# Performance work log

Hardware: AMD Instinct MI355X
Metric: run time of the kernel (lower is better)

The kernel has to match this reference:

```python
import jax, jax.numpy as jnp
import numpy as np

B, S, H, NH = 4, 1024, 1024, 16
HD = H // NH
I = 4096
EPS = 1e-12
BASE = 10000.0


def setup_inputs() -> dict:
    key = jax.random.key(0)
    ks = jax.random.split(key, 6)
    sc = 0.02
    return {
        "x": jax.random.normal(ks[0], (B, S, H), jnp.float32),
        "ln1_w": jnp.ones((H,), jnp.float32),
        "ln1_b": jnp.zeros((H,), jnp.float32),
        "qkv_w": jax.random.normal(ks[1], (3 * H, H), jnp.float32) * sc,
        "qkv_b": jnp.zeros((3 * H,), jnp.float32),
        "out_w": jax.random.normal(ks[2], (H, H), jnp.float32) * sc,
        "out_b": jnp.zeros((H,), jnp.float32),
        "ln2_w": jnp.ones((H,), jnp.float32),
        "ln2_b": jnp.zeros((H,), jnp.float32),
        "i2h_w": jax.random.normal(ks[3], (2 * I, H), jnp.float32) * sc,
        "i2h_b": jnp.zeros((2 * I,), jnp.float32),
        "h2o_w": jax.random.normal(ks[4], (H, I), jnp.float32) * sc,
        "h2o_b": jnp.zeros((H,), jnp.float32),
    }


def _layer_norm(x, w, b, eps=EPS):
    mu = jnp.mean(x, axis=-1, keepdims=True)
    var = jnp.mean(jnp.square(x - mu), axis=-1, keepdims=True)
    return (x - mu) * jax.lax.rsqrt(var + eps) * w + b


def _rope_cos_sin(seq_len, dim, base):
    # inv_freq = base ** linspace(0, -1 + 2/dim, dim//2), repeated twice
    half = jnp.power(base, jnp.linspace(0.0, -1.0 + 2.0 / dim, dim // 2, dtype=jnp.float32))
    inv_freq = jnp.concatenate([half, half])  # [dim]
    t = jnp.arange(seq_len, dtype=jnp.float32)
    freqs = t[:, None] * inv_freq[None, :]  # [seq, dim]
    return jnp.cos(freqs), jnp.sin(freqs)


def _rotate(x, cos, sin):
    # x: [B, NH, S, HD]; cos/sin: [S, HD]
    xl, xr = jnp.split(x, 2, axis=-1)
    x_rot = jnp.concatenate([-xr, xl], axis=-1)
    return x * cos + x_rot * sin


def _forward(x, ln1_w, ln1_b, qkv_w, qkv_b, out_w, out_b,
             ln2_w, ln2_b, i2h_w, i2h_b, h2o_w, h2o_b):
    b, s, h = x.shape
    # --- LeanSelfAttention (pre-LN, rotary, causal, residual) ---
    h_ln = _layer_norm(x, ln1_w, ln1_b)
    qkv = h_ln @ qkv_w.T + qkv_b  # [b, s, 3h]
    q, k, v = jnp.split(qkv, 3, axis=-1)
    to_heads = lambda t: t.reshape(b, s, NH, HD).transpose(0, 2, 1, 3)  # [b,nh,s,hd]
    q, k, v = to_heads(q), to_heads(k), to_heads(v)
    cos, sin = _rope_cos_sin(s, HD, BASE)
    q, k = _rotate(q, cos, sin), _rotate(k, cos, sin)
    scores = jnp.einsum("bhqd,bhkd->bhqk", q, k) / np.sqrt(HD).astype(np.float32)
    causal = jnp.tril(jnp.ones((s, s), dtype=bool))
    scores = jnp.where(causal, scores, jnp.float32(-10000.0))
    probs = jax.nn.softmax(scores, axis=-1)
    attn = jnp.einsum("bhqk,bhkd->bhqd", probs, v)
    attn = attn.transpose(0, 2, 1, 3).reshape(b, s, h)
    attn_out = attn @ out_w.T + out_b + x  # residual
    # --- LeanFFN (pre-LN, gated gelu, residual) ---
    ffn_ln = _layer_norm(attn_out, ln2_w, ln2_b)
    pre = ffn_ln @ i2h_w.T + i2h_b  # [b, s, 2I]
    gate, lin = jnp.split(pre, 2, axis=-1)
    hid = jax.nn.gelu(gate, approximate=False) * lin
    return hid @ h2o_w.T + h2o_b + attn_out


def reference(x, ln1_w, ln1_b, qkv_w, qkv_b, out_w, out_b,
              ln2_w, ln2_b, i2h_w, i2h_b, h2o_w, h2o_b):
    return _forward(x, ln1_w, ln1_b, qkv_w, qkv_b, out_w, out_b,
                    ln2_w, ln2_b, i2h_w, i2h_b, h2o_w, h2o_b)
```

## Files before the change

kernel.cpp:

```cpp
#include <hip/hip_runtime.h>
#include <cstdint>
#include <cstddef>

typedef __bf16 bf16;
typedef __bf16 bf16x4 __attribute__((ext_vector_type(4)));
typedef __bf16 bf16x8 __attribute__((ext_vector_type(8)));
typedef float  f32x4  __attribute__((ext_vector_type(4)));

#define GLD16(gptr, lptr)                                                      \
  __builtin_amdgcn_global_load_lds(                                            \
      (__attribute__((address_space(1))) unsigned int*)(gptr),                 \
      (__attribute__((address_space(3))) unsigned int*)(lptr), 16, 0, 0)

__global__ __launch_bounds__(256)
void convert_kernel(const float* __restrict__ src, bf16* __restrict__ dst, int n8)
{
    const int j = blockIdx.x * 256 + threadIdx.x;
    if (j >= n8) return;
    const float* s = src + (size_t)j * 8;
    bf16x8 o;
#pragma unroll
    for (int e = 0; e < 8; ++e) o[e] = (bf16)s[e];
    ((bf16x8*)dst)[j] = o;
}

template<class InT>
__global__ __launch_bounds__(256)
void ln_kernel(const InT* __restrict__ x, const float* __restrict__ w,
               const float* __restrict__ b, bf16* __restrict__ out)
{
    __shared__ float red[8];
    const int row = blockIdx.x;
    const int tid = threadIdx.x;
    const InT* xr = x + (size_t)row * 1024;
    float xf[4], s = 0.f, ss = 0.f;
#pragma unroll
    for (int j = 0; j < 4; ++j) {
        xf[j] = (float)xr[tid * 4 + j];
        s += xf[j]; ss += xf[j] * xf[j];
    }
#pragma unroll
    for (int off = 32; off > 0; off >>= 1) { s += __shfl_xor(s, off); ss += __shfl_xor(ss, off); }
    if ((tid & 63) == 0) { red[(tid >> 6) * 2] = s; red[(tid >> 6) * 2 + 1] = ss; }
    __syncthreads();
    s  = red[0] + red[2] + red[4] + red[6];
    ss = red[1] + red[3] + red[5] + red[7];
    const float mu   = s * (1.f / 1024.f);
    const float var  = ss * (1.f / 1024.f) - mu * mu;
    const float rstd = rsqrtf(var + 1e-12f);
    bf16x4 ov;
#pragma unroll
    for (int j = 0; j < 4; ++j)
        ov[j] = (bf16)((xf[j] - mu) * rstd * w[tid * 4 + j] + b[tid * 4 + j]);
    *(bf16x4*)(out + (size_t)row * 1024 + tid * 4) = ov;
}

template<int RES_MODE, bool OUT_F32>
__global__ __launch_bounds__(256)
void gemm_bt(const bf16* __restrict__ A, const bf16* __restrict__ W,
             const float* __restrict__ bias, const void* __restrict__ res,
             void* __restrict__ Cv, int M, int N, int K)
{
    __shared__ alignas(16) bf16 As[128][32];
    __shared__ alignas(16) bf16 Bs[128][32];
    const int tid  = threadIdx.x;
    const int lane = tid & 63, wid = tid >> 6;
    const int lr = lane & 15, lg = lane >> 4;
    const int kgrp = lg * 8;
    const int wm = (wid >> 1) * 64, wn = (wid & 1) * 64;
    const int row0 = blockIdx.x * 128, col0 = blockIdx.y * 128;

    f32x4 acc[4][4] = {};

    for (int k0 = 0; k0 < K; k0 += 32) {
#pragma unroll
        for (int i = 0; i < 2; ++i) {
            const int c = i * 256 + tid;
            const int r = c >> 2, k8 = (c & 3) * 8;
            GLD16(A + (size_t)(row0 + r) * K + k0 + k8,
                  (char*)&As[0][0] + (size_t)(i * 256 + wid * 64) * 16);
            GLD16(W + (size_t)(col0 + r) * K + k0 + k8,
                  (char*)&Bs[0][0] + (size_t)(i * 256 + wid * 64) * 16);
        }
        __syncthreads();
        bf16x8 af[4], bw[4];
#pragma unroll
        for (int mi = 0; mi < 4; ++mi) af[mi] = *(const bf16x8*)&As[wm + mi * 16 + lr][kgrp];
#pragma unroll
        for (int ni = 0; ni < 4; ++ni) bw[ni] = *(const bf16x8*)&Bs[wn + ni * 16 + lr][kgrp];
#pragma unroll
        for (int mi = 0; mi < 4; ++mi)
#pragma unroll
            for (int ni = 0; ni < 4; ++ni)
                acc[mi][ni] = __builtin_amdgcn_mfma_f32_16x16x32_bf16(
                    af[mi], bw[ni], acc[mi][ni], 0, 0, 0);
        __syncthreads();
    }

#pragma unroll
    for (int ni = 0; ni < 4; ++ni) {
        const int ccol = col0 + wn + ni * 16 + lr;
        const float bv = bias[ccol];
#pragma unroll
        for (int mi = 0; mi < 4; ++mi)
#pragma unroll
            for (int r = 0; r < 4; ++r) {
                const size_t crow = (size_t)(row0 + wm + mi * 16 + lg * 4 + r);
                float v = acc[mi][ni][r] + bv;
                if constexpr (RES_MODE == 1) v += ((const float*)res)[crow * N + ccol];
                if constexpr (RES_MODE == 2) v += (float)((const bf16*)res)[crow * N + ccol];
                if constexpr (OUT_F32) ((float*)Cv)[crow * N + ccol] = v;
                else                   ((bf16*)Cv)[crow * N + ccol] = (bf16)v;
            }
    }
}

__global__ __launch_bounds__(256)
void gemm_qkv_rope(const bf16* __restrict__ A, const bf16* __restrict__ W,
                   const float* __restrict__ bias, bf16* __restrict__ q_r,
                   bf16* __restrict__ k_r, bf16* __restrict__ v_r)
{
    __shared__ alignas(16) bf16 As[128][32];
    __shared__ alignas(16) bf16 Bs[128][32];
    const int tid  = threadIdx.x;
    const int lane = tid & 63, wid = tid >> 6;
    const int lr = lane & 15, lg = lane >> 4;
    const int kgrp = lg * 8;
    const int wm = (wid >> 1) * 64, wn = (wid & 1) * 64;
    const int row0 = blockIdx.x * 128, col0 = blockIdx.y * 128;
    const int K = 1024;

    f32x4 acc[4][4] = {};

    for (int k0 = 0; k0 < K; k0 += 32) {
#pragma unroll
        for (int i = 0; i < 2; ++i) {
            const int c = i * 256 + tid;
            const int r = c >> 2, k8 = (c & 3) * 8;
            GLD16(A + (size_t)(row0 + r) * K + k0 + k8,
                  (char*)&As[0][0] + (size_t)(i * 256 + wid * 64) * 16);
            GLD16(W + (size_t)(col0 + r) * K + k0 + k8,
                  (char*)&Bs[0][0] + (size_t)(i * 256 + wid * 64) * 16);
        }
        __syncthreads();
        bf16x8 af[4], bw[4];
#pragma unroll
        for (int mi = 0; mi < 4; ++mi) af[mi] = *(const bf16x8*)&As[wm + mi * 16 + lr][kgrp];
#pragma unroll
        for (int ni = 0; ni < 4; ++ni) bw[ni] = *(const bf16x8*)&Bs[wn + ni * 16 + lr][kgrp];
#pragma unroll
        for (int mi = 0; mi < 4; ++mi)
#pragma unroll
            for (int ni = 0; ni < 4; ++ni)
                acc[mi][ni] = __builtin_amdgcn_mfma_f32_16x16x32_bf16(
                    af[mi], bw[ni], acc[mi][ni], 0, 0, 0);
        __syncthreads();
    }

    const int third = blockIdx.y >> 3;
    bf16* dst = (third == 0) ? q_r : (third == 1) ? k_r : v_r;
#pragma unroll
    for (int ni = 0; ni < 2; ++ni) {
        const int i_ = ni * 16 + lr;
        const int ccol = col0 + wn + ni * 16 + lr;
        const int h = (ccol >> 6) & 15;
        const float blo = bias[ccol], bhi = bias[ccol + 32];
        const float inv = __expf((float)i_ * (-9.210340371976184f / 32.f));
#pragma unroll
        for (int mi = 0; mi < 4; ++mi)
#pragma unroll
            for (int r = 0; r < 4; ++r) {
                const int crow = row0 + wm + mi * 16 + lg * 4 + r;
                const int s = crow & 1023, b = crow >> 10;
                const float lo = acc[mi][ni][r] + blo;
                const float hi = acc[mi][ni + 2][r] + bhi;
                const size_t ob = ((size_t)(b * 16 + h) * 1024 + s) * 64;
                if (third == 2) {
                    dst[ob + i_]      = (bf16)lo;
                    dst[ob + i_ + 32] = (bf16)hi;
                } else {
                    float sn, c;
                    sincosf((float)s * inv, &sn, &c);
                    dst[ob + i_]      = (bf16)(lo * c - hi * sn);
                    dst[ob + i_ + 32] = (bf16)(hi * c + lo * sn);
                }
            }
    }
}

__global__ __launch_bounds__(512, 2)
void gemm_i2h_g8(const bf16* __restrict__ A, const bf16* __restrict__ W,
                 const float* __restrict__ bias, bf16* __restrict__ hid)
{
    __shared__ alignas(16) char smem[3 * 32768];
    const int tid  = threadIdx.x;
    const int lane = tid & 63, wid = tid >> 6;
    const int lrr  = lane & 15, lg = lane >> 4;
    const int wr = wid >> 2, wc = wid & 3;
    const int row0 = blockIdx.x * 256;
    const int colh = blockIdx.y * 128 + wc * 32;
    const int NT = 32;

    const int cA0 = tid, cA1 = 512 + tid;
    const int rA0 = cA0 >> 2, rA1 = cA1 >> 2, rB = tid >> 2;
    const int swA0 = (((cA0 & 3) * 16) ^ (((rA0 >> 1) & 3) << 4)) >> 1;
    const int swA1 = (((cA1 & 3) * 16) ^ (((rA1 >> 1) & 3) << 4)) >> 1;
    const int swB  = (((tid & 3) * 16) ^ (((rB  >> 1) & 3) << 4)) >> 1;
    const bf16* gA0 = A + (size_t)(row0 + rA0) * 1024 + swA0;
    const bf16* gA1 = A + (size_t)(row0 + rA1) * 1024 + swA1;
    const bf16* gBg = W + (size_t)(blockIdx.y * 128 + rB) * 1024 + swB;
    const bf16* gBl = W + (size_t)(4096 + blockIdx.y * 128 + rB) * 1024 + swB;
    const int dA0 = (wid * 64) * 16, dA1 = (512 + wid * 64) * 16, dB = (wid * 64) * 16;

    f32x4 acc[8][4] = {};

    {
        char* b0 = smem;
        GLD16(gBg, b0 + 16384 + dB); GLD16(gBl, b0 + 24576 + dB);
        GLD16(gA0, b0 + dA0);        GLD16(gA1, b0 + dA1);
        char* b1 = smem + 32768;
        GLD16(gBg + 32, b1 + 16384 + dB); GLD16(gBl + 32, b1 + 24576 + dB);
        GLD16(gA0 + 32, b1 + dA0);        GLD16(gA1 + 32, b1 + dA1);
    }
    asm volatile("s_waitcnt vmcnt(4)\ns_barrier" ::: "memory");

    int cur = 0, stg = 2;
    for (int t = 0; t < NT; ++t) {
        const char* bA  = smem + cur * 32768;
        const char* bBg = bA + 16384;
        const char* bBl = bA + 24576;
        char* sB = smem + stg * 32768;
        const int k0s = (t + 2) * 32;
        const bool dostg = (t < NT - 2);

        if (dostg) { GLD16(gBg + k0s, sB + 16384 + dB); GLD16(gBl + k0s, sB + 24576 + dB); }
        bf16x8 bf[4], af[4];
        const int bcol = lg * 16;
#pragma unroll
        for (int nv = 0; nv < 4; ++nv) {
            const int row = wc * 32 + (nv & 1) * 16 + lrr;
            const char* base = (nv < 2) ? bBg : bBl;
            bf[nv] = *(const bf16x8*)(base + row * 64 + (bcol ^ (((row >> 1) & 3) << 4)));
        }
#pragma unroll
        for (int mi = 0; mi < 4; ++mi) {
            const int row = wr * 128 + mi * 16 + lrr;
            af[mi] = *(const bf16x8*)(bA + row * 64 + (bcol ^ (((row >> 1) & 3) << 4)));
        }
        __builtin_amdgcn_s_barrier();
        __builtin_amdgcn_s_setprio(1);
#pragma unroll
        for (int mi = 0; mi < 4; ++mi)
#pragma unroll
            for (int nv = 0; nv < 4; ++nv)
                acc[mi][nv] = __builtin_amdgcn_mfma_f32_16x16x32_bf16(
                    af[mi], bf[nv], acc[mi][nv], 0, 0, 0);
        __builtin_amdgcn_s_setprio(0);
        __builtin_amdgcn_s_barrier();

        if (dostg) { GLD16(gA0 + k0s, sB + dA0); GLD16(gA1 + k0s, sB + dA1); }
#pragma unroll
        for (int mi = 0; mi < 4; ++mi) {
            const int row = wr * 128 + (4 + mi) * 16 + lrr;
            af[mi] = *(const bf16x8*)(bA + row * 64 + (bcol ^ (((row >> 1) & 3) << 4)));
        }
        __builtin_amdgcn_s_barrier();
        __builtin_amdgcn_s_setprio(1);
#pragma unroll
        for (int mi = 0; mi < 4; ++mi)
#pragma unroll
            for (int nv = 0; nv < 4; ++nv)
                acc[4 + mi][nv] = __builtin_amdgcn_mfma_f32_16x16x32_bf16(
                    af[mi], bf[nv], acc[4 + mi][nv], 0, 0, 0);
        __builtin_amdgcn_s_setprio(0);

        if (dostg) asm volatile("s_waitcnt vmcnt(4)\ns_barrier" ::: "memory");
        else       asm volatile("s_waitcnt vmcnt(0)\ns_barrier" ::: "memory");
        cur = (cur == 2) ? 0 : cur + 1;
        stg = (stg == 2) ? 0 : stg + 1;
    }

#pragma unroll
    for (int c = 0; c < 2; ++c) {
        const int gcol = colh + c * 16 + lrr;
        const float bg_ = bias[gcol], bl_ = bias[4096 + gcol];
#pragma unroll
        for (int mi = 0; mi < 8; ++mi)
#pragma unroll
            for (int r = 0; r < 4; ++r) {
                const size_t row = (size_t)(row0 + wr * 128 + mi * 16 + lg * 4 + r);
                const float g = acc[mi][c][r] + bg_;
                const float l = acc[mi][2 + c][r] + bl_;
                const float ge = 0.5f * g * (1.f + erff(g * 0.70710678118654752f));
                hid[row * 4096 + gcol] = (bf16)(ge * l);
            }
    }
}

__global__ __launch_bounds__(256)
void attn_kernel(const bf16* __restrict__ q_r, const bf16* __restrict__ k_r,
                 const bf16* __restrict__ v_r, bf16* __restrict__ attn)
{
    __shared__ alignas(16) bf16 Ks[64][72];
    __shared__ alignas(16) bf16 Vt[64][72];
    __shared__ alignas(16) bf16 Ps[4][16][72];
    const int qt = blockIdx.x, bh = blockIdx.y;
    const int tid = threadIdx.x, lane = tid & 63, w = tid >> 6;
    const int lr = lane & 15, lg = lane >> 4;
    const int kgrp = lg * 8;
    const int qbase = qt * 64;

    const bf16* qrow = q_r + ((size_t)bh * 1024 + qbase + w * 16 + lr) * 64;
    const bf16x8 qf0 = *(const bf16x8*)(qrow + kgrp);
    const bf16x8 qf1 = *(const bf16x8*)(qrow + 32 + kgrp);

    f32x4 o[4] = {};
    float m_r[4], l_r[4];
#pragma unroll
    for (int r = 0; r < 4; ++r) { m_r[r] = -1e30f; l_r[r] = 0.f; }

    const int nchunk = qt + 1;
    for (int ic = 0; ic < nchunk; ++ic) {
        const int kb = ic * 64;
        __syncthreads();
#pragma unroll
        for (int i = 0; i < 2; ++i) {
            const int c = i * 256 + tid;
            const int row = c >> 3, e8 = (c & 7) * 8;
            *(bf16x8*)&Ks[row][e8] =
                *(const bf16x8*)(k_r + ((size_t)bh * 1024 + kb + row) * 64 + e8);
            const bf16x8 vv =
                *(const bf16x8*)(v_r + ((size_t)bh * 1024 + kb + row) * 64 + e8);
#pragma unroll
            for (int j = 0; j < 8; ++j) Vt[e8 + j][row] = vv[j];
        }
        __syncthreads();

        f32x4 sv[4] = {};
#pragma unroll
        for (int nb = 0; nb < 4; ++nb) {
            const bf16x8 kf0 = *(const bf16x8*)&Ks[nb * 16 + lr][kgrp];
            const bf16x8 kf1 = *(const bf16x8*)&Ks[nb * 16 + lr][32 + kgrp];
            sv[nb] = __builtin_amdgcn_mfma_f32_16x16x32_bf16(qf0, kf0, sv[nb], 0, 0, 0);
            sv[nb] = __builtin_amdgcn_mfma_f32_16x16x32_bf16(qf1, kf1, sv[nb], 0, 0, 0);
        }

        const bool diag = (kb == qbase);
        float pv[4][4];
#pragma unroll
        for (int r = 0; r < 4; ++r) {
            float s0[4];
#pragma unroll
            for (int nb = 0; nb < 4; ++nb) {
                float t = sv[nb][r] * 0.125f;
                if (diag && (nb * 16 + lr) > (w * 16 + lg * 4 + r)) t = -10000.f;
                s0[nb] = t;
            }
            float rm = fmaxf(fmaxf(s0[0], s0[1]), fmaxf(s0[2], s0[3]));
#pragma unroll
            for (int off = 1; off < 16; off <<= 1) rm = fmaxf(rm, __shfl_xor(rm, off));
            const float nm = fmaxf(m_r[r], rm);
            const float sc = __expf(m_r[r] - nm);
            float rs = 0.f;
#pragma unroll
            for (int nb = 0; nb < 4; ++nb) {
                const float p = __expf(s0[nb] - nm);
                pv[nb][r] = p; rs += p;
            }
#pragma unroll
            for (int off = 1; off < 16; off <<= 1) rs += __shfl_xor(rs, off);
            l_r[r] = l_r[r] * sc + rs;
            m_r[r] = nm;
#pragma unroll
            for (int nb = 0; nb < 4; ++nb) o[nb][r] *= sc;
        }

#pragma unroll
        for (int nb = 0; nb < 4; ++nb)
#pragma unroll
            for (int r = 0; r < 4; ++r)
                Ps[w][lg * 4 + r][nb * 16 + lr] = (bf16)pv[nb][r];
#pragma unroll
        for (int nb = 0; nb < 4; ++nb)
#pragma unroll
            for (int ks = 0; ks < 2; ++ks) {
                const bf16x8 pa = *(const bf16x8*)&Ps[w][lr][ks * 32 + kgrp];
                const bf16x8 vb = *(const bf16x8*)&Vt[nb * 16 + lr][ks * 32 + kgrp];
                o[nb] = __builtin_amdgcn_mfma_f32_16x16x32_bf16(pa, vb, o[nb], 0, 0, 0);
            }
    }

    const int b = bh >> 4, head = bh & 15;
#pragma unroll
    for (int nb = 0; nb < 4; ++nb)
#pragma unroll
        for (int r = 0; r < 4; ++r) {
            const size_t rw = (size_t)(b * 1024 + qbase + w * 16 + lg * 4 + r);
            attn[rw * 1024 + head * 64 + nb * 16 + lr] = (bf16)(o[nb][r] / l_r[r]);
        }
}

extern "C" void kernel_launch(void* const* d_in, const int* in_sizes, int n_in,
                              void* d_out, int out_size, void* d_ws, size_t ws_size,
                              hipStream_t stream)
{
    const float* x    = (const float*)d_in[0];
    const float* ln1w = (const float*)d_in[1];
    const float* ln1b = (const float*)d_in[2];
    const float* qkvw = (const float*)d_in[3];
    const float* qkvb = (const float*)d_in[4];
    const float* outw = (const float*)d_in[5];
    const float* outb = (const float*)d_in[6];
    const float* ln2w = (const float*)d_in[7];
    const float* ln2b = (const float*)d_in[8];
    const float* i2hw = (const float*)d_in[9];
    const float* i2hb = (const float*)d_in[10];
    const float* h2ow = (const float*)d_in[11];
    const float* h2ob = (const float*)d_in[12];

    char* ws = (char*)d_ws;
    const size_t MB = 1024 * 1024;

    bf16* h_ln    = (bf16*)(ws + 0);
    bf16* q_r     = (bf16*)(ws + 8 * MB);
    bf16* k_r     = (bf16*)(ws + 16 * MB);
    bf16* v_r     = (bf16*)(ws + 24 * MB);
    bf16* attn    = (bf16*)(ws + 32 * MB);
    bf16* attnout = (bf16*)(ws + 40 * MB);
    bf16* ffnln   = (bf16*)(ws + 48 * MB);
    bf16* hid     = (bf16*)(ws + 56 * MB);
    bf16* qkvw_c  = (bf16*)(ws + 88 * MB);
    bf16* outw_c  = (bf16*)(ws + 94 * MB);
    bf16* i2hw_c  = (bf16*)(ws + 96 * MB);
    bf16* h2ow_c  = (bf16*)(ws + 112 * MB);

    convert_kernel<<<1536, 256, 0, stream>>>(qkvw, qkvw_c, 3145728 / 8);
    convert_kernel<<< 512, 256, 0, stream>>>(outw, outw_c, 1048576 / 8);
    convert_kernel<<<4096, 256, 0, stream>>>(i2hw, i2hw_c, 8388608 / 8);
    convert_kernel<<<2048, 256, 0, stream>>>(h2ow, h2ow_c, 4194304 / 8);

    ln_kernel<float><<<4096, 256, 0, stream>>>(x, ln1w, ln1b, h_ln);
    gemm_qkv_rope<<<dim3(32, 24), 256, 0, stream>>>(h_ln, qkvw_c, qkvb,
                                                    q_r, k_r, v_r);
    attn_kernel<<<dim3(16, 64), 256, 0, stream>>>(q_r, k_r, v_r, attn);
    gemm_bt<1, false><<<dim3(32, 8), 256, 0, stream>>>(
        attn, outw_c, outb, x, attnout, 4096, 1024, 1024);
    ln_kernel<bf16><<<4096, 256, 0, stream>>>(attnout, ln2w, ln2b, ffnln);
    gemm_i2h_g8<<<dim3(16, 32), 512, 0, stream>>>(ffnln, i2hw_c, i2hb, hid);
    gemm_bt<2, true><<<dim3(32, 8), 256, 0, stream>>>(
        hid, h2ow_c, h2ob, attnout, d_out, 4096, 1024, 4096);
}
```

Before: 484.9 us.

## Split-K the h2o GEMM into four partial passes plus a reduction kernel

The final h2o projection (K=4096) previously ran on a 32x8 grid of only 256 blocks. It is now split along K into four 1024-wide slices written as fp32 partials, followed by a reduction kernel that adds bias and residual. This raises block count to 1024 to fill more CUs, at the cost of 64MB of partial writes and reads. It also folds the 1/sqrt(d) scale into Q inside the QKV epilogue, removing a multiply per score in attention.

```diff
diff --git a/kernel.cpp b/kernel.cpp
--- a/kernel.cpp
+++ b/kernel.cpp
@@ -116,6 +116,83 @@
 }
 
 __global__ __launch_bounds__(256)
+void gemm_h2o_sk(const bf16* __restrict__ A, const bf16* __restrict__ W,
+                 float* __restrict__ part)
+{
+    __shared__ alignas(16) bf16 As[128][32];
+    __shared__ alignas(16) bf16 Bs[128][32];
+    const int tid  = threadIdx.x;
+    const int lane = tid & 63, wid = tid >> 6;
+    const int lr = lane & 15, lg = lane >> 4;
+    const int kgrp = lg * 8;
+    const int wm = (wid >> 1) * 64, wn = (wid & 1) * 64;
+    const int row0 = blockIdx.x * 128, col0 = blockIdx.y * 128;
+    const int kbase = blockIdx.z * 1024;
+    const int K = 4096;
+
+    f32x4 acc[4][4] = {};
+
+    for (int k0 = kbase; k0 < kbase + 1024; k0 += 32) {
+#pragma unroll
+        for (int i = 0; i < 2; ++i) {
+            const int c = i * 256 + tid;
+            const int r = c >> 2, k8 = (c & 3) * 8;
+            GLD16(A + (size_t)(row0 + r) * K + k0 + k8,
+                  (char*)&As[0][0] + (size_t)(i * 256 + wid * 64) * 16);
+            GLD16(W + (size_t)(col0 + r) * K + k0 + k8,
+                  (char*)&Bs[0][0] + (size_t)(i * 256 + wid * 64) * 16);
+        }
+        __syncthreads();
+        bf16x8 af[4], bw[4];
+#pragma unroll
+        for (int mi = 0; mi < 4; ++mi) af[mi] = *(const bf16x8*)&As[wm + mi * 16 + lr][kgrp];
+#pragma unroll
+        for (int ni = 0; ni < 4; ++ni) bw[ni] = *(const bf16x8*)&Bs[wn + ni * 16 + lr][kgrp];
+#pragma unroll
+        for (int mi = 0; mi < 4; ++mi)
+#pragma unroll
+            for (int ni = 0; ni < 4; ++ni)
+                acc[mi][ni] = __builtin_amdgcn_mfma_f32_16x16x32_bf16(
+                    af[mi], bw[ni], acc[mi][ni], 0, 0, 0);
+        __syncthreads();
+    }
+
+    float* dst = part + (size_t)blockIdx.z * 4096 * 1024;
+#pragma unroll
+    for (int ni = 0; ni < 4; ++ni) {
+        const int ccol = col0 + wn + ni * 16 + lr;
+#pragma unroll
+        for (int mi = 0; mi < 4; ++mi)
+#pragma unroll
+            for (int r = 0; r < 4; ++r) {
+                const size_t crow = (size_t)(row0 + wm + mi * 16 + lg * 4 + r);
+                dst[crow * 1024 + ccol] = acc[mi][ni][r];
+            }
+    }
+}
+
+__global__ __launch_bounds__(256)
+void h2o_reduce(const float* __restrict__ part, const float* __restrict__ bias,
+                const bf16* __restrict__ res, float* __restrict__ out)
+{
+    const size_t g = ((size_t)blockIdx.x * 256 + threadIdx.x) * 4;
+    const int col = (int)(g & 1023);
+    f32x4 v = *(const f32x4*)(part + g);
+#pragma unroll
+    for (int s = 1; s < 4; ++s) {
+        const f32x4 p = *(const f32x4*)(part + (size_t)s * 4096 * 1024 + g);
+#pragma unroll
+        for (int j = 0; j < 4; ++j) v[j] += p[j];
+    }
+    const f32x4 bv = *(const f32x4*)(bias + col);
+    const bf16x4 rv = *(const bf16x4*)(res + g);
+    f32x4 o;
+#pragma unroll
+    for (int j = 0; j < 4; ++j) o[j] = v[j] + bv[j] + (float)rv[j];
+    *(f32x4*)(out + g) = o;
+}
+
+__global__ __launch_bounds__(256)
 void gemm_qkv_rope(const bf16* __restrict__ A, const bf16* __restrict__ W,
                    const float* __restrict__ bias, bf16* __restrict__ q_r,
                    bf16* __restrict__ k_r, bf16* __restrict__ v_r)
@@ -159,6 +236,7 @@
 
     const int third = blockIdx.y >> 3;
     bf16* dst = (third == 0) ? q_r : (third == 1) ? k_r : v_r;
+    const float qs = (third == 0) ? 0.125f : 1.f;
 #pragma unroll
     for (int ni = 0; ni < 2; ++ni) {
         const int i_ = ni * 16 + lr;
@@ -181,8 +259,8 @@
                 } else {
                     float sn, c;
                     sincosf((float)s * inv, &sn, &c);
-                    dst[ob + i_]      = (bf16)(lo * c - hi * sn);
-                    dst[ob + i_ + 32] = (bf16)(hi * c + lo * sn);
+                    dst[ob + i_]      = (bf16)((lo * c - hi * sn) * qs);
+                    dst[ob + i_ + 32] = (bf16)((hi * c + lo * sn) * qs);
                 }
             }
     }
@@ -352,7 +430,7 @@
             float s0[4];
 #pragma unroll
             for (int nb = 0; nb < 4; ++nb) {
-                float t = sv[nb][r] * 0.125f;
+                float t = sv[nb][r];
                 if (diag && (nb * 16 + lr) > (w * 16 + lg * 4 + r)) t = -10000.f;
                 s0[nb] = t;
             }
@@ -421,18 +499,19 @@
     char* ws = (char*)d_ws;
     const size_t MB = 1024 * 1024;
 
-    bf16* h_ln    = (bf16*)(ws + 0);
-    bf16* q_r     = (bf16*)(ws + 8 * MB);
-    bf16* k_r     = (bf16*)(ws + 16 * MB);
-    bf16* v_r     = (bf16*)(ws + 24 * MB);
-    bf16* attn    = (bf16*)(ws + 32 * MB);
-    bf16* attnout = (bf16*)(ws + 40 * MB);
-    bf16* ffnln   = (bf16*)(ws + 48 * MB);
-    bf16* hid     = (bf16*)(ws + 56 * MB);
-    bf16* qkvw_c  = (bf16*)(ws + 88 * MB);
-    bf16* outw_c  = (bf16*)(ws + 94 * MB);
-    bf16* i2hw_c  = (bf16*)(ws + 96 * MB);
-    bf16* h2ow_c  = (bf16*)(ws + 112 * MB);
+    bf16*  h_ln    = (bf16*)(ws + 0);
+    bf16*  q_r     = (bf16*)(ws + 8 * MB);
+    bf16*  k_r     = (bf16*)(ws + 16 * MB);
+    bf16*  v_r     = (bf16*)(ws + 24 * MB);
+    bf16*  attn    = (bf16*)(ws + 32 * MB);
+    bf16*  ffnln   = (bf16*)(ws + 40 * MB);
+    float* part    = (float*)(ws + 0);
+    bf16*  attnout = (bf16*)(ws + 64 * MB);
+    bf16*  hid     = (bf16*)(ws + 72 * MB);
+    bf16*  qkvw_c  = (bf16*)(ws + 104 * MB);
+    bf16*  outw_c  = (bf16*)(ws + 110 * MB);
+    bf16*  i2hw_c  = (bf16*)(ws + 112 * MB);
+    bf16*  h2ow_c  = (bf16*)(ws + 128 * MB);
 
     convert_kernel<<<1536, 256, 0, stream>>>(qkvw, qkvw_c, 3145728 / 8);
     convert_kernel<<< 512, 256, 0, stream>>>(outw, outw_c, 1048576 / 8);
@@ -447,6 +526,6 @@
         attn, outw_c, outb, x, attnout, 4096, 1024, 1024);
     ln_kernel<bf16><<<4096, 256, 0, stream>>>(attnout, ln2w, ln2b, ffnln);
     gemm_i2h_g8<<<dim3(16, 32), 512, 0, stream>>>(ffnln, i2hw_c, i2hb, hid);
-    gemm_bt<2, true><<<dim3(32, 8), 256, 0, stream>>>(
-        hid, h2ow_c, h2ob, attnout, d_out, 4096, 1024, 4096);
-}
+    gemm_h2o_sk<<<dim3(32, 8, 4), 256, 0, stream>>>(hid, h2ow_c, part);
+    h2o_reduce<<<4096, 256, 0, stream>>>(part, h2ob, attnout, (float*)d_out);
+}
```

New measurement: 473.1 us. 1.03x faster.
